# Performance work log

Measured on AMD Instinct MI355X. Metric: run time of the kernel, lower is better.

Reference implementation:

```python
import jax, jax.numpy as jnp
import numpy as np

D_MODEL = 2048
D_INNER = 4096   # expand * d_model == ngroups * d_state
D_XB = 1024
N_HEADS = 32     # = ngroups
HEAD_DIM = 128   # = d_state
N_KV_HEADS = D_XB // HEAD_DIM  # 8
N_REP = N_HEADS // N_KV_HEADS  # 4
D_IN_PROJ = D_INNER + 2 * D_XB + D_INNER + N_HEADS  # 10272
ROPE_BASE = 10000.0


def setup_inputs() -> dict:
    key = jax.random.key(0)
    k1, k2, k3 = jax.random.split(key, 3)
    u = jax.random.normal(k1, (2, 2048, D_MODEL), dtype=jnp.float32)
    W_in = jax.random.normal(k2, (D_IN_PROJ, D_MODEL), dtype=jnp.float32) * (1.0 / np.sqrt(D_MODEL))
    W_out = jax.random.normal(k3, (D_MODEL, D_INNER), dtype=jnp.float32) * (1.0 / np.sqrt(D_INNER))
    return {"u": u, "W_in": W_in, "W_out": W_out}


def _rotate_half(x):
    x1, x2 = jnp.split(x, 2, axis=-1)
    return jnp.concatenate((-x2, x1), axis=-1)


def _rope_cos_sin(seqlen, dim, dtype):
    inv_freq = 1.0 / (ROPE_BASE ** (jnp.arange(0, dim, 2, dtype=jnp.float32) / dim))
    pos = jnp.arange(seqlen, dtype=jnp.float32)
    freqs = pos[:, None] * inv_freq[None, :]          # [S, dim/2]
    emb = jnp.concatenate((freqs, freqs), axis=-1)    # [S, dim]
    return jnp.cos(emb).astype(dtype), jnp.sin(emb).astype(dtype)


def reference(u, W_in, W_out):
    # NOTE: the module's forward short-circuits (early return) into a GQA
    # attention path; the SSM code after the return is dead.
    B, S, _ = u.shape
    zxbcdt = jnp.einsum('bsd,ed->bse', u, W_in)       # [B, S, D_IN_PROJ]
    # split: z (d_inner), x (d_xb), B (d_xb), C (d_inner), dt (nheads); d_mlp = 0
    o0 = D_INNER
    x = zxbcdt[..., o0:o0 + D_XB]
    Bm = zxbcdt[..., o0 + D_XB:o0 + 2 * D_XB]
    C = zxbcdt[..., o0 + 2 * D_XB:o0 + 2 * D_XB + D_INNER]
    # q = C (32 heads), k = B (8 heads), v = x (8 heads); [B, H, S, Dh]
    q = C.reshape(B, S, N_HEADS, HEAD_DIM).transpose(0, 2, 1, 3)
    k = Bm.reshape(B, S, N_KV_HEADS, HEAD_DIM).transpose(0, 2, 1, 3)
    v = x.reshape(B, S, N_KV_HEADS, HEAD_DIM).transpose(0, 2, 1, 3)
    cos, sin = _rope_cos_sin(S, HEAD_DIM, u.dtype)    # [S, Dh]
    cos = cos[None, None]                             # [1, 1, S, Dh]
    sin = sin[None, None]
    q = q * cos + _rotate_half(q) * sin
    k = k * cos + _rotate_half(k) * sin
    # repeat_kv: repeat_interleave along head dim
    k = jnp.repeat(k, N_REP, axis=1)
    v = jnp.repeat(v, N_REP, axis=1)
    scale = 1.0 / np.sqrt(HEAD_DIM)
    scores = jnp.einsum('bhqd,bhkd->bhqk', q, k) * scale
    causal = jnp.tril(jnp.ones((S, S), dtype=bool))
    scores = jnp.where(causal[None, None], scores, jnp.finfo(scores.dtype).min)
    attn = jax.nn.softmax(scores, axis=-1)
    out = jnp.einsum('bhqk,bhkd->bhqd', attn, v)      # [B, H, S, Dh]
    out = out.transpose(0, 2, 1, 3).reshape(B, S, D_INNER)
    return jnp.einsum('bse,de->bsd', out, W_out)      # [B, S, d_model]
```

## Files before the change

### kernel.cpp

```cpp
#include <hip/hip_runtime.h>
#include <stdint.h>

#define S_LEN 2048
#define BATCH 2
#define NH 32
#define NKV 8
#define HD 128
#define NE 6144

typedef __attribute__((ext_vector_type(8))) short short8;
typedef __attribute__((ext_vector_type(4))) float floatx4;

__device__ __forceinline__ unsigned short f2bf(float f) {
    union { float f; uint32_t u; } v; v.f = f;
    uint32_t u = v.u;
    u += 0x7FFFu + ((u >> 16) & 1u);
    return (unsigned short)(u >> 16);
}
__device__ __forceinline__ float bf2f(unsigned short h) {
    union { uint32_t u; float f; } v; v.u = ((uint32_t)h) << 16;
    return v.f;
}

__global__ void cast_f32_bf16(const float* __restrict__ in,
                              unsigned short* __restrict__ out, int n4) {
    int i = blockIdx.x * blockDim.x + threadIdx.x;
    if (i >= n4) return;
    float4 f = reinterpret_cast<const float4*>(in)[i];
    ushort4 o;
    o.x = f2bf(f.x); o.y = f2bf(f.y); o.z = f2bf(f.z); o.w = f2bf(f.w);
    reinterpret_cast<ushort4*>(out)[i] = o;
}

template <int OUT_BF16>
__global__ void __launch_bounds__(256)
gemm_bt(const unsigned short* __restrict__ A, const unsigned short* __restrict__ Bt,
        void* __restrict__ Cv, int M, int N, int K) {
    __shared__ unsigned short As[128 * 32];
    __shared__ unsigned short Bs[128 * 32];
    const int tid  = threadIdx.x;
    const int w    = tid >> 6;
    const int lane = tid & 63;
    const int quad = lane >> 4;
    const int l16  = lane & 15;
    const int wm   = w >> 1, wn = w & 1;
    const int m0 = blockIdx.y * 128, n0 = blockIdx.x * 128;

    floatx4 acc[4][4];
#pragma unroll
    for (int i = 0; i < 4; i++)
#pragma unroll
        for (int j = 0; j < 4; j++) acc[i][j] = {0.f, 0.f, 0.f, 0.f};

    const int lr = lane >> 2;
    const int lk = (lane & 3) * 8;
    const int KT = K >> 5;

    for (int kt = 0; kt < KT; ++kt) {
        const int k0 = kt << 5;
        __syncthreads();
#pragma unroll
        for (int c = 0; c < 2; ++c) {
            const int chunk = w * 2 + c;
            const unsigned short* ga = A  + (size_t)(m0 + chunk * 16 + lr) * K + k0 + lk;
            __builtin_amdgcn_global_load_lds(
                (const __attribute__((address_space(1))) void*)ga,
                (__attribute__((address_space(3))) void*)(As + chunk * 512), 16, 0, 0);
            const unsigned short* gb = Bt + (size_t)(n0 + chunk * 16 + lr) * K + k0 + lk;
            __builtin_amdgcn_global_load_lds(
                (const __attribute__((address_space(1))) void*)gb,
                (__attribute__((address_space(3))) void*)(Bs + chunk * 512), 16, 0, 0);
        }
        __syncthreads();
        short8 af[4], bf[4];
#pragma unroll
        for (int t = 0; t < 4; ++t) {
            af[t] = *reinterpret_cast<const short8*>(As + (wm * 64 + t * 16 + l16) * 32 + quad * 8);
            bf[t] = *reinterpret_cast<const short8*>(Bs + (wn * 64 + t * 16 + l16) * 32 + quad * 8);
        }
#pragma unroll
        for (int i = 0; i < 4; i++)
#pragma unroll
            for (int j = 0; j < 4; j++)
                acc[i][j] = __builtin_amdgcn_mfma_f32_16x16x32_bf16(af[i], bf[j], acc[i][j], 0, 0, 0);
    }

#pragma unroll
    for (int i = 0; i < 4; i++)
#pragma unroll
        for (int j = 0; j < 4; j++) {
            const int row = m0 + wm * 64 + i * 16 + quad * 4;
            const int col = n0 + wn * 64 + j * 16 + l16;
#pragma unroll
            for (int r = 0; r < 4; r++) {
                float vv = acc[i][j][r];
                if (OUT_BF16)
                    ((unsigned short*)Cv)[(size_t)(row + r) * N + col] = f2bf(vv);
                else
                    ((float*)Cv)[(size_t)(row + r) * N + col] = vv;
            }
        }
}

#define QSCALE 0.12748539509360f
__global__ void rope_split(const unsigned short* __restrict__ Z,
                           unsigned short* __restrict__ Q,
                           unsigned short* __restrict__ Kb,
                           unsigned short* __restrict__ Vt) {
    const int PER_TOK = 2048 + 512 + 1024;
    int idx = blockIdx.x * blockDim.x + threadIdx.x;
    if (idx >= BATCH * S_LEN * PER_TOK) return;
    int t = idx / PER_TOK;
    int r = idx - t * PER_TOK;
    int b = t / S_LEN, s = t - b * S_LEN;
    const unsigned short* z = Z + (size_t)t * NE;
    if (r < 2048) {
        int h = r >> 6, j = r & 63;
        float x0 = bf2f(z[2048 + h * 128 + j]);
        float x1 = bf2f(z[2048 + h * 128 + j + 64]);
        float inv = exp2f((float)j * -0.20762050593f);
        float c, sn; sincosf((float)s * inv, &sn, &c);
        size_t base = ((size_t)(b * NH + h) * S_LEN + s) * HD;
        Q[base + j]      = f2bf((x0 * c - x1 * sn) * QSCALE);
        Q[base + j + 64] = f2bf((x1 * c + x0 * sn) * QSCALE);
    } else if (r < 2560) {
        int rr = r - 2048; int kh = rr >> 6, j = rr & 63;
        float x0 = bf2f(z[1024 + kh * 128 + j]);
        float x1 = bf2f(z[1024 + kh * 128 + j + 64]);
        float inv = exp2f((float)j * -0.20762050593f);
        float c, sn; sincosf((float)s * inv, &sn, &c);
        size_t base = ((size_t)(b * NKV + kh) * S_LEN + s) * HD;
        Kb[base + j]      = f2bf(x0 * c - x1 * sn);
        Kb[base + j + 64] = f2bf(x1 * c + x0 * sn);
    } else {
        int m = r - 2560; int kh = m >> 7, d = m & 127;
        Vt[((size_t)(b * NKV + kh) * HD + d) * S_LEN + s] = z[m];
    }
}

__global__ void __launch_bounds__(256)
attn_kernel(const unsigned short* __restrict__ Q,
            const unsigned short* __restrict__ Kb,
            const unsigned short* __restrict__ Vt,
            unsigned short* __restrict__ Ob) {
    __shared__ unsigned short Ks[64 * 128];
    __shared__ unsigned short Vs[128 * 64];
    __shared__ unsigned short Ps[4][16 * 64];
    const int tid  = threadIdx.x;
    const int w    = tid >> 6;
    const int lane = tid & 63;
    const int quad = lane >> 4;
    const int l16  = lane & 15;
    const int blk = blockIdx.x;
    const int qt = 31 - (blk >> 6);
    const int bh = blk & 63;
    const int h = bh & 31, b = bh >> 5;
    const int kvh = h >> 2;
    const int qw0 = qt * 64 + w * 16;

    const unsigned short* Qbase = Q  + ((size_t)(b * NH  + h)   * S_LEN) * HD;
    const unsigned short* Kbase = Kb + ((size_t)(b * NKV + kvh) * S_LEN) * HD;
    const unsigned short* Vbase = Vt + ((size_t)(b * NKV + kvh) * HD) * S_LEN;

    short8 qf[4];
    {
        const unsigned short* qrow = Qbase + (size_t)(qw0 + l16) * HD + quad * 8;
#pragma unroll
        for (int ks = 0; ks < 4; ++ks)
            qf[ks] = *reinterpret_cast<const short8*>(qrow + ks * 32);
    }

    floatx4 oacc[8];
#pragma unroll
    for (int i = 0; i < 8; i++) oacc[i] = {0.f, 0.f, 0.f, 0.f};
    float lsum[4] = {0.f, 0.f, 0.f, 0.f};

    const int s_row = (lane >> 4);
    const int k_pc  = lane & 15;
    const int v_pc  = lane & 7;
    const int kv_end = qt * 64 + 64;

    for (int kv0 = 0; kv0 < kv_end; kv0 += 64) {
        __syncthreads();
#pragma unroll
        for (int c = 0; c < 4; ++c) {
            const int bI = w * 4 + c;
            const int row = bI * 4 + s_row;
            const int lc = k_pc ^ (row & 7);
            const unsigned short* ga = Kbase + (size_t)(kv0 + row) * HD + lc * 8;
            __builtin_amdgcn_global_load_lds(
                (const __attribute__((address_space(1))) void*)ga,
                (__attribute__((address_space(3))) void*)(Ks + bI * 512), 16, 0, 0);
        }
#pragma unroll
        for (int c = 0; c < 4; ++c) {
            const int bI = w * 4 + c;
            const int drow = bI * 8 + (lane >> 3);
            const int lc = v_pc ^ (drow & 7);
            const unsigned short* ga = Vbase + (size_t)drow * S_LEN + kv0 + lc * 8;
            __builtin_amdgcn_global_load_lds(
                (const __attribute__((address_space(1))) void*)ga,
                (__attribute__((address_space(3))) void*)(Vs + bI * 512), 16, 0, 0);
        }
        __syncthreads();

        if (kv0 <= qw0 + 15) {
            const bool diag = (kv0 + 63 > qw0);
            floatx4 sacc[4];
#pragma unroll
            for (int nt = 0; nt < 4; nt++) sacc[nt] = {0.f, 0.f, 0.f, 0.f};
#pragma unroll
            for (int ks = 0; ks < 4; ++ks) {
#pragma unroll
                for (int nt = 0; nt < 4; ++nt) {
                    const int srow = nt * 16 + l16;
                    const int pc = (ks * 4 + quad) ^ (l16 & 7);
                    short8 kf = *reinterpret_cast<const short8*>(Ks + srow * 128 + pc * 8);
                    sacc[nt] = __builtin_amdgcn_mfma_f32_16x16x32_bf16(qf[ks], kf, sacc[nt], 0, 0, 0);
                }
            }
            unsigned short* pw = &Ps[w][0];
#pragma unroll
            for (int nt = 0; nt < 4; ++nt) {
                const int col = kv0 + nt * 16 + l16;
                const int cch = nt * 2 + (l16 >> 3);
#pragma unroll
                for (int r = 0; r < 4; ++r) {
                    const int row = qw0 + quad * 4 + r;
                    float p = (!diag || col <= row) ? exp2f(sacc[nt][r]) : 0.0f;
                    lsum[r] += p;
                    const int prow = quad * 4 + r;
                    const int pc = cch ^ (prow & 7);
                    pw[prow * 64 + pc * 8 + (l16 & 7)] = f2bf(p);
                }
            }
#pragma unroll
            for (int kv_sub = 0; kv_sub < 2; ++kv_sub) {
                const int pcP = (kv_sub * 4 + quad) ^ (l16 & 7);
                short8 pf = *reinterpret_cast<const short8*>(pw + l16 * 64 + pcP * 8);
#pragma unroll
                for (int dt = 0; dt < 8; ++dt) {
                    const int drow = dt * 16 + l16;
                    const int pcV = (kv_sub * 4 + quad) ^ (l16 & 7);
                    short8 vf = *reinterpret_cast<const short8*>(Vs + drow * 64 + pcV * 8);
                    oacc[dt] = __builtin_amdgcn_mfma_f32_16x16x32_bf16(pf, vf, oacc[dt], 0, 0, 0);
                }
            }
        }
    }

    float linv[4];
#pragma unroll
    for (int r = 0; r < 4; ++r) {
        float s = lsum[r];
#pragma unroll
        for (int off = 1; off < 16; off <<= 1) s += __shfl_xor(s, off);
        linv[r] = 1.0f / s;
    }
#pragma unroll
    for (int dt = 0; dt < 8; ++dt) {
        const int d = dt * 16 + l16;
#pragma unroll
        for (int r = 0; r < 4; ++r) {
            const int row = qw0 + quad * 4 + r;
            Ob[((size_t)(b * S_LEN + row)) * 4096 + h * 128 + d] = f2bf(oacc[dt][r] * linv[r]);
        }
    }
}

extern "C" void kernel_launch(void* const* d_in, const int* in_sizes, int n_in,
                              void* d_out, int out_size, void* d_ws, size_t ws_size,
                              hipStream_t stream) {
    const float* u     = (const float*)d_in[0];
    const float* W_in  = (const float*)d_in[1];
    const float* W_out = (const float*)d_in[2];
    float* out = (float*)d_out;

    char* ws = (char*)d_ws;
    unsigned short* u_bf    = (unsigned short*)(ws);
    unsigned short* win_bf  = (unsigned short*)(ws + 16777216);
    unsigned short* wout_bf = (unsigned short*)(ws + 41943040);
    unsigned short* Z       = (unsigned short*)(ws + 58720256);
    unsigned short* Qb      = (unsigned short*)(ws + 109051904);
    unsigned short* Kv      = (unsigned short*)(ws + 142606336);
    unsigned short* Vt      = (unsigned short*)(ws + 150994944);
    unsigned short* Ob      = (unsigned short*)(ws + 159383552);

    {
        int n4 = (2 * 2048 * 2048) / 4;
        cast_f32_bf16<<<(n4 + 255) / 256, 256, 0, stream>>>(u, u_bf, n4);
        n4 = (6144 * 2048) / 4;
        cast_f32_bf16<<<(n4 + 255) / 256, 256, 0, stream>>>(W_in + (size_t)4096 * 2048, win_bf, n4);
        n4 = (2048 * 4096) / 4;
        cast_f32_bf16<<<(n4 + 255) / 256, 256, 0, stream>>>(W_out, wout_bf, n4);
    }
    {
        dim3 g(6144 / 128, 4096 / 128);
        gemm_bt<1><<<g, 256, 0, stream>>>(u_bf, win_bf, Z, 4096, 6144, 2048);
    }
    {
        int n = BATCH * S_LEN * 3584;
        rope_split<<<(n + 255) / 256, 256, 0, stream>>>(Z, Qb, Kv, Vt);
    }
    attn_kernel<<<BATCH * NH * (S_LEN / 64), 256, 0, stream>>>(Qb, Kv, Vt, Ob);
    {
        dim3 g(2048 / 128, 4096 / 128);
        gemm_bt<0><<<g, 256, 0, stream>>>(Ob, wout_bf, out, 4096, 2048, 4096);
    }
}
```

Before: 559.4 us.

## Enlarge attention query tile to 128 rows and read V directly from global

Each attention block now covers 128 query rows, and each wave handles two 16-row query tiles, so every staged K tile is reused across twice as many queries and K staging traffic is halved. The S MFMA operands are swapped so scores come out transposed, which lets probabilities be packed into bf16 pairs and written as 8-byte stores. V is no longer staged in LDS and is read per-lane from global memory, which removes LDS traffic and the V staging but relies on cache hits for repeated reads. The grid is halved, so fewer blocks are available to fill the GPU, causal imbalance grows, and register pressure rises from the doubled accumulators.

New measurement: 649.3 us. +16.1%, slower.

```diff
diff --git a/kernel.cpp b/kernel.cpp
--- a/kernel.cpp
+++ b/kernel.cpp
@@ -20,6 +20,13 @@
 __device__ __forceinline__ float bf2f(unsigned short h) {
     union { uint32_t u; float f; } v; v.u = ((uint32_t)h) << 16;
     return v.f;
+}
+__device__ __forceinline__ uint32_t rtn_u(float f) {
+    union { float f; uint32_t u; } v; v.f = f;
+    return v.u + 0x7FFFu + ((v.u >> 16) & 1u);
+}
+__device__ __forceinline__ uint32_t pack_bf2(float a, float b) {
+    return __builtin_amdgcn_perm(rtn_u(b), rtn_u(a), 0x07060302);
 }
 
 __global__ void cast_f32_bf16(const float* __restrict__ in,
@@ -144,126 +151,141 @@
             const unsigned short* __restrict__ Vt,
             unsigned short* __restrict__ Ob) {
     __shared__ unsigned short Ks[64 * 128];
-    __shared__ unsigned short Vs[128 * 64];
-    __shared__ unsigned short Ps[4][16 * 64];
+    __shared__ unsigned short Ps[4][32 * 64];
     const int tid  = threadIdx.x;
     const int w    = tid >> 6;
     const int lane = tid & 63;
     const int quad = lane >> 4;
     const int l16  = lane & 15;
     const int blk = blockIdx.x;
-    const int qt = 31 - (blk >> 6);
+    const int qt = 15 - (blk >> 6);
     const int bh = blk & 63;
     const int h = bh & 31, b = bh >> 5;
     const int kvh = h >> 2;
-    const int qw0 = qt * 64 + w * 16;
+    const int q0blk = qt * 128;
+    const int wq0 = q0blk + w * 32;
 
     const unsigned short* Qbase = Q  + ((size_t)(b * NH  + h)   * S_LEN) * HD;
     const unsigned short* Kbase = Kb + ((size_t)(b * NKV + kvh) * S_LEN) * HD;
     const unsigned short* Vbase = Vt + ((size_t)(b * NKV + kvh) * HD) * S_LEN;
 
-    short8 qf[4];
-    {
-        const unsigned short* qrow = Qbase + (size_t)(qw0 + l16) * HD + quad * 8;
+    short8 qf[2][4];
+#pragma unroll
+    for (int q_t = 0; q_t < 2; ++q_t) {
+        const unsigned short* qrow = Qbase + (size_t)(wq0 + q_t * 16 + l16) * HD + quad * 8;
 #pragma unroll
         for (int ks = 0; ks < 4; ++ks)
-            qf[ks] = *reinterpret_cast<const short8*>(qrow + ks * 32);
-    }
-
-    floatx4 oacc[8];
-#pragma unroll
-    for (int i = 0; i < 8; i++) oacc[i] = {0.f, 0.f, 0.f, 0.f};
-    float lsum[4] = {0.f, 0.f, 0.f, 0.f};
-
-    const int s_row = (lane >> 4);
-    const int k_pc  = lane & 15;
-    const int v_pc  = lane & 7;
-    const int kv_end = qt * 64 + 64;
+            qf[q_t][ks] = *reinterpret_cast<const short8*>(qrow + ks * 32);
+    }
+
+    floatx4 oacc[2][8];
+#pragma unroll
+    for (int q_t = 0; q_t < 2; ++q_t)
+#pragma unroll
+        for (int dt = 0; dt < 8; ++dt) oacc[q_t][dt] = {0.f, 0.f, 0.f, 0.f};
+    float lsum[2] = {0.f, 0.f};
+
+    const int stg_row = lane >> 4;
+    const int stg_pc  = lane & 15;
+    unsigned short* pw = &Ps[w][0];
+    const int e2 = (l16 & 7) << 1;
+    const int kv_end = q0blk + 128;
 
     for (int kv0 = 0; kv0 < kv_end; kv0 += 64) {
         __syncthreads();
 #pragma unroll
         for (int c = 0; c < 4; ++c) {
             const int bI = w * 4 + c;
-            const int row = bI * 4 + s_row;
-            const int lc = k_pc ^ (row & 7);
+            const int row = bI * 4 + stg_row;
+            const int lc = stg_pc ^ (row & 7);
             const unsigned short* ga = Kbase + (size_t)(kv0 + row) * HD + lc * 8;
             __builtin_amdgcn_global_load_lds(
                 (const __attribute__((address_space(1))) void*)ga,
                 (__attribute__((address_space(3))) void*)(Ks + bI * 512), 16, 0, 0);
         }
-#pragma unroll
-        for (int c = 0; c < 4; ++c) {
-            const int bI = w * 4 + c;
-            const int drow = bI * 8 + (lane >> 3);
-            const int lc = v_pc ^ (drow & 7);
-            const unsigned short* ga = Vbase + (size_t)drow * S_LEN + kv0 + lc * 8;
-            __builtin_amdgcn_global_load_lds(
-                (const __attribute__((address_space(1))) void*)ga,
-                (__attribute__((address_space(3))) void*)(Vs + bI * 512), 16, 0, 0);
-        }
         __syncthreads();
 
-        if (kv0 <= qw0 + 15) {
-            const bool diag = (kv0 + 63 > qw0);
-            floatx4 sacc[4];
-#pragma unroll
-            for (int nt = 0; nt < 4; nt++) sacc[nt] = {0.f, 0.f, 0.f, 0.f};
+        if (kv0 < wq0 + 32) {
+            const bool diag = (kv0 + 63 > wq0);
+            floatx4 sacc[2][4];
+#pragma unroll
+            for (int q_t = 0; q_t < 2; ++q_t)
+#pragma unroll
+                for (int mt = 0; mt < 4; ++mt) sacc[q_t][mt] = {0.f, 0.f, 0.f, 0.f};
 #pragma unroll
             for (int ks = 0; ks < 4; ++ks) {
 #pragma unroll
-                for (int nt = 0; nt < 4; ++nt) {
-                    const int srow = nt * 16 + l16;
-                    const int pc = (ks * 4 + quad) ^ (l16 & 7);
-                    short8 kf = *reinterpret_cast<const short8*>(Ks + srow * 128 + pc * 8);
-                    sacc[nt] = __builtin_amdgcn_mfma_f32_16x16x32_bf16(qf[ks], kf, sacc[nt], 0, 0, 0);
+                for (int mt = 0; mt < 4; ++mt) {
+                    const int row = mt * 16 + l16;
+                    const int slot = (ks * 4 + quad) ^ (l16 & 7);
+                    short8 kf = *reinterpret_cast<const short8*>(Ks + row * 128 + slot * 8);
+#pragma unroll
+                    for (int q_t = 0; q_t < 2; ++q_t)
+                        sacc[q_t][mt] = __builtin_amdgcn_mfma_f32_16x16x32_bf16(
+                            kf, qf[q_t][ks], sacc[q_t][mt], 0, 0, 0);
                 }
             }
-            unsigned short* pw = &Ps[w][0];
-#pragma unroll
-            for (int nt = 0; nt < 4; ++nt) {
-                const int col = kv0 + nt * 16 + l16;
-                const int cch = nt * 2 + (l16 >> 3);
-#pragma unroll
-                for (int r = 0; r < 4; ++r) {
-                    const int row = qw0 + quad * 4 + r;
-                    float p = (!diag || col <= row) ? exp2f(sacc[nt][r]) : 0.0f;
-                    lsum[r] += p;
-                    const int prow = quad * 4 + r;
-                    const int pc = cch ^ (prow & 7);
-                    pw[prow * 64 + pc * 8 + (l16 & 7)] = f2bf(p);
+#pragma unroll
+            for (int q_t = 0; q_t < 2; ++q_t) {
+                const int qrow = wq0 + q_t * 16 + l16;
+                const int prow = q_t * 16 + l16;
+#pragma unroll
+                for (int mt = 0; mt < 4; ++mt) {
+                    const int kvb = kv0 + mt * 16 + quad * 4;
+                    float p0 = exp2f(sacc[q_t][mt][0]);
+                    float p1 = exp2f(sacc[q_t][mt][1]);
+                    float p2 = exp2f(sacc[q_t][mt][2]);
+                    float p3 = exp2f(sacc[q_t][mt][3]);
+                    if (diag) {
+                        p0 = (kvb + 0 <= qrow) ? p0 : 0.f;
+                        p1 = (kvb + 1 <= qrow) ? p1 : 0.f;
+                        p2 = (kvb + 2 <= qrow) ? p2 : 0.f;
+                        p3 = (kvb + 3 <= qrow) ? p3 : 0.f;
+                    }
+                    lsum[q_t] += (p0 + p1) + (p2 + p3);
+                    const int phys = (mt * 4 + quad) ^ e2;
+                    uint2 pk; pk.x = pack_bf2(p0, p1); pk.y = pack_bf2(p2, p3);
+                    *reinterpret_cast<uint2*>(pw + prow * 64 + phys * 4) = pk;
                 }
             }
 #pragma unroll
-            for (int kv_sub = 0; kv_sub < 2; ++kv_sub) {
-                const int pcP = (kv_sub * 4 + quad) ^ (l16 & 7);
-                short8 pf = *reinterpret_cast<const short8*>(pw + l16 * 64 + pcP * 8);
+            for (int kp = 0; kp < 2; ++kp) {
+                short8 pf[2];
+#pragma unroll
+                for (int q_t = 0; q_t < 2; ++q_t) {
+                    const int phys = (kp * 8 + quad * 2) ^ e2;
+                    pf[q_t] = *reinterpret_cast<const short8*>(
+                        pw + (q_t * 16 + l16) * 64 + phys * 4);
+                }
+                const unsigned short* vp = Vbase + (size_t)l16 * S_LEN + kv0 + kp * 32 + quad * 8;
 #pragma unroll
                 for (int dt = 0; dt < 8; ++dt) {
-                    const int drow = dt * 16 + l16;
-                    const int pcV = (kv_sub * 4 + quad) ^ (l16 & 7);
-                    short8 vf = *reinterpret_cast<const short8*>(Vs + drow * 64 + pcV * 8);
-                    oacc[dt] = __builtin_amdgcn_mfma_f32_16x16x32_bf16(pf, vf, oacc[dt], 0, 0, 0);
+                    short8 vf = *reinterpret_cast<const short8*>(vp + (size_t)dt * 16 * S_LEN);
+#pragma unroll
+                    for (int q_t = 0; q_t < 2; ++q_t)
+                        oacc[q_t][dt] = __builtin_amdgcn_mfma_f32_16x16x32_bf16(
+                            pf[q_t], vf, oacc[q_t][dt], 0, 0, 0);
                 }
             }
         }
     }
 
-    float linv[4];
-#pragma unroll
-    for (int r = 0; r < 4; ++r) {
-        float s = lsum[r];
-#pragma unroll
-        for (int off = 1; off < 16; off <<= 1) s += __shfl_xor(s, off);
-        linv[r] = 1.0f / s;
-    }
-#pragma unroll
-    for (int dt = 0; dt < 8; ++dt) {
-        const int d = dt * 16 + l16;
+#pragma unroll
+    for (int q_t = 0; q_t < 2; ++q_t) {
+        float s = lsum[q_t];
+        s += __shfl_xor(s, 16);
+        s += __shfl_xor(s, 32);
+        float linv = 1.0f / s;
 #pragma unroll
         for (int r = 0; r < 4; ++r) {
-            const int row = qw0 + quad * 4 + r;
-            Ob[((size_t)(b * S_LEN + row)) * 4096 + h * 128 + d] = f2bf(oacc[dt][r] * linv[r]);
+            const float lr = __shfl(linv, quad * 4 + r);
+            const int row = wq0 + q_t * 16 + quad * 4 + r;
+#pragma unroll
+            for (int dt = 0; dt < 8; ++dt) {
+                const int d = dt * 16 + l16;
+                Ob[((size_t)(b * S_LEN + row)) * 4096 + h * 128 + d] =
+                    f2bf(oacc[q_t][dt][r] * lr);
+            }
         }
     }
 }
@@ -302,7 +324,7 @@
         int n = BATCH * S_LEN * 3584;
         rope_split<<<(n + 255) / 256, 256, 0, stream>>>(Z, Qb, Kv, Vt);
     }
-    attn_kernel<<<BATCH * NH * (S_LEN / 64), 256, 0, stream>>>(Qb, Kv, Vt, Ob);
+    attn_kernel<<<BATCH * NH * (S_LEN / 128), 256, 0, stream>>>(Qb, Kv, Vt, Ob);
     {
         dim3 g(2048 / 128, 4096 / 128);
         gemm_bt<0><<<g, 256, 0, stream>>>(Ob, wout_bf, out, 4096, 2048, 4096);
```
